# Kernel tuning notes

Measured on AMD Instinct MI355X. Metric: run time of the kernel, lower is better.

The kernel has to match this reference:

```python
import jax, jax.numpy as jnp
import numpy as np

D_MODEL = 512
H = 8
D_FF = 2048
EPS = 1e-6
NEG_INF = -1.0e9


def setup_inputs() -> dict:
    key = jax.random.key(0)
    ks = jax.random.split(key, 12)
    B, S, D, F = 8, 2048, D_MODEL, D_FF
    s = 0.02
    inp = {
        "x": jax.random.normal(ks[0], (B, S, D), jnp.float32),
        "src_mask": jnp.ones((B, 1, 1, S), jnp.int32),
        "w_q": jax.random.normal(ks[1], (D, D), jnp.float32) * s,
        "b_q": jnp.zeros((D,), jnp.float32),
        "w_k": jax.random.normal(ks[2], (D, D), jnp.float32) * s,
        "b_k": jnp.zeros((D,), jnp.float32),
        "w_v": jax.random.normal(ks[3], (D, D), jnp.float32) * s,
        "b_v": jnp.zeros((D,), jnp.float32),
        "w_o": jax.random.normal(ks[4], (D, D), jnp.float32) * s,
        "b_o": jnp.zeros((D,), jnp.float32),
        "w_1": jax.random.normal(ks[5], (F, D), jnp.float32) * s,
        "b_1": jnp.zeros((F,), jnp.float32),
        "w_2": jax.random.normal(ks[6], (D, F), jnp.float32) * s,
        "b_2": jnp.zeros((D,), jnp.float32),
    }
    return inp


def _layer_norm(x):
    # Matches torch: (x - mu) / sqrt(std**2 + eps), std is UNBIASED (ddof=1);
    # alpha/bias params exist in the module but are never applied in forward.
    mu = jnp.mean(x, axis=-1, keepdims=True)
    var = jnp.var(x, axis=-1, keepdims=True, ddof=1)
    return (x - mu) / jnp.sqrt(var + EPS)


def _mha(x, src_mask, w_q, b_q, w_k, b_k, w_v, b_v, w_o, b_o):
    B, S, D = x.shape
    d_k = D // H
    q = x @ w_q.T + b_q
    k = x @ w_k.T + b_k
    v = x @ w_v.T + b_v
    # (B, S, H, d_k) -> (B, H, S, d_k)
    q = q.reshape(B, S, H, d_k).transpose(0, 2, 1, 3)
    k = k.reshape(B, S, H, d_k).transpose(0, 2, 1, 3)
    v = v.reshape(B, S, H, d_k).transpose(0, 2, 1, 3)
    scores = jnp.einsum("bhqd,bhkd->bhqk", q, k) / jnp.sqrt(jnp.float32(d_k))
    scores = jnp.where(src_mask == 0, NEG_INF, scores)
    attn = jax.nn.softmax(scores, axis=-1)  # (B, H, S, S) materialized, as in source
    out = jnp.einsum("bhqk,bhkd->bhqd", attn, v)
    out = out.transpose(0, 2, 1, 3).reshape(B, S, D)
    return out @ w_o.T + b_o


def _ffn(x, w_1, b_1, w_2, b_2):
    return jax.nn.relu(x @ w_1.T + b_1) @ w_2.T + b_2


def reference(x, src_mask, w_q, b_q, w_k, b_k, w_v, b_v, w_o, b_o, w_1, b_1, w_2, b_2):
    # dropout prob = 0.0 -> identity (eval-equivalent)
    x1 = x + _mha(_layer_norm(x), src_mask, w_q, b_q, w_k, b_k, w_v, b_v, w_o, b_o)
    return x1 + _ffn(_layer_norm(x1), w_1, b_1, w_2, b_2)
```

## Files before the change

kernel.cpp:

```cpp
#include <hip/hip_runtime.h>
#include <hip/hip_bf16.h>

typedef unsigned short u16;
typedef __bf16 bf16x8 __attribute__((ext_vector_type(8)));
typedef unsigned int u32x4 __attribute__((ext_vector_type(4)));
typedef float f32x4 __attribute__((ext_vector_type(4)));

#define SEQ 2048
#define DMODEL 512
#define NHEAD 8
#define DFF 2048
#define NBATCH 8
#define MROWS (NBATCH * SEQ)

#define C1_FOLD 0.18033688f

__device__ __forceinline__ u16 f2b(float f) {
    __hip_bfloat16 h = __float2bfloat16(f);
    u16 u;
    __builtin_memcpy(&u, &h, 2);
    return u;
}

__device__ __forceinline__ unsigned int pack2(float a, float b) {
    float2 f{a, b};
    __hip_bfloat162 h = __float22bfloat162_rn(f);
    unsigned int u;
    __builtin_memcpy(&u, &h, 4);
    return u;
}

__device__ __forceinline__ float ex2(float x) {
#if __has_builtin(__builtin_amdgcn_exp2f)
    return __builtin_amdgcn_exp2f(x);
#else
    return exp2f(x);
#endif
}

__device__ __forceinline__ void gload_lds16(const void* g, void* lds) {
    auto* gp = reinterpret_cast<const __attribute__((address_space(1))) unsigned int*>(
        reinterpret_cast<uintptr_t>(g));
    auto* lp = reinterpret_cast<__attribute__((address_space(3))) unsigned int*>(
        reinterpret_cast<uintptr_t>(lds));
    __builtin_amdgcn_global_load_lds(gp, lp, 16, 0, 0);
}

__global__ __launch_bounds__(256) void cast_weights(
    const float* __restrict__ w0, const float* __restrict__ w1,
    const float* __restrict__ w2, const float* __restrict__ w3,
    const float* __restrict__ w4, const float* __restrict__ w5,
    u16* __restrict__ d0, u16* __restrict__ d1, u16* __restrict__ d2,
    u16* __restrict__ d3, u16* __restrict__ d4, u16* __restrict__ d5) {
    int blk = blockIdx.x;
    const float* s;
    u16* d;
    int base;
    float sc = 1.0f;
    if (blk < 512) {
        int seg = blk >> 7, lb = blk & 127;
        s = seg == 0 ? w0 : seg == 1 ? w1 : seg == 2 ? w2 : w3;
        d = seg == 0 ? d0 : seg == 1 ? d1 : seg == 2 ? d2 : d3;
        base = lb * 2048;
        if (seg == 0) sc = C1_FOLD;
    } else if (blk < 1024) {
        s = w4; d = d4; base = (blk - 512) * 2048;
    } else {
        s = w5; d = d5; base = (blk - 1024) * 2048;
    }
    int i = base + threadIdx.x * 8;
    float4 a = *reinterpret_cast<const float4*>(s + i);
    float4 b = *reinterpret_cast<const float4*>(s + i + 4);
    ushort4 oa, ob;
    oa.x = f2b(a.x * sc); oa.y = f2b(a.y * sc);
    oa.z = f2b(a.z * sc); oa.w = f2b(a.w * sc);
    ob.x = f2b(b.x * sc); ob.y = f2b(b.y * sc);
    ob.z = f2b(b.z * sc); ob.w = f2b(b.w * sc);
    *reinterpret_cast<ushort4*>(d + i) = oa;
    *reinterpret_cast<ushort4*>(d + i + 4) = ob;
}

__global__ __launch_bounds__(256) void concat_bias(const float* __restrict__ bq,
                                                   const float* __restrict__ bk,
                                                   const float* __restrict__ bv,
                                                   float* __restrict__ dst) {
    int i = blockIdx.x * 256 + threadIdx.x;
    float v = i < 512 ? bq[i] * C1_FOLD : (i < 1024 ? bk[i - 512] : bv[i - 1024]);
    dst[i] = v;
}

__global__ __launch_bounds__(256) void ln_rows(const float* __restrict__ x,
                                               u16* __restrict__ out) {
    int row = blockIdx.x * 4 + (threadIdx.x >> 6);
    int l = threadIdx.x & 63;
    const float* xr = x + (size_t)row * DMODEL + l * 8;
    float4 a = *reinterpret_cast<const float4*>(xr);
    float4 b = *reinterpret_cast<const float4*>(xr + 4);
    float s = a.x + a.y + a.z + a.w + b.x + b.y + b.z + b.w;
    float q = a.x * a.x + a.y * a.y + a.z * a.z + a.w * a.w +
              b.x * b.x + b.y * b.y + b.z * b.z + b.w * b.w;
#pragma unroll
    for (int d = 32; d >= 1; d >>= 1) {
        s += __shfl_xor(s, d, 64);
        q += __shfl_xor(q, d, 64);
    }
    float mean = s * (1.f / 512.f);
    float var = (q - 512.f * mean * mean) * (1.f / 511.f);
    float rs = rsqrtf(var + 1e-6f);
    ushort4 o0, o1;
    o0.x = f2b((a.x - mean) * rs); o0.y = f2b((a.y - mean) * rs);
    o0.z = f2b((a.z - mean) * rs); o0.w = f2b((a.w - mean) * rs);
    o1.x = f2b((b.x - mean) * rs); o1.y = f2b((b.y - mean) * rs);
    o1.z = f2b((b.z - mean) * rs); o1.w = f2b((b.w - mean) * rs);
    u16* op = out + (size_t)row * DMODEL + l * 8;
    *reinterpret_cast<ushort4*>(op) = o0;
    *reinterpret_cast<ushort4*>(op + 4) = o1;
}

template <bool RELU, bool RESID, int OUTMODE>
__global__ __launch_bounds__(256, 2) void gemm_nt(
    const u16* __restrict__ A, const u16* __restrict__ W,
    const float* __restrict__ bias, const float* __restrict__ resid,
    void* __restrict__ Cout, void* __restrict__ Cout2, int N, int K) {
    __shared__ u16 Als[2][128 * 64];
    __shared__ u16 Bls[2][128 * 64];
    const int tid = threadIdx.x;
    const int l = tid & 63, w = tid >> 6;
    const int m0 = blockIdx.y * 128;
    const int n0 = blockIdx.x * 128;
    const int wr = (w >> 1) * 64, wc = (w & 1) * 64;
    const int lhi = l >> 4, l15 = l & 15, l7 = l & 7;

    f32x4 acc[4][4] = {};

    const int srow = l >> 3;
    const int scol = ((l & 7) * 8) ^ (srow << 3);

    auto stage = [&](int buf, int kt) {
#pragma unroll
        for (int i = 0; i < 4; ++i) {
            int cc = w * 4 + i;
            int grow = cc * 8 + srow;
            gload_lds16(&A[(size_t)(m0 + grow) * K + kt + scol],
                        &Als[buf][cc * 512]);
            gload_lds16(&W[(size_t)(n0 + grow) * K + kt + scol],
                        &Bls[buf][cc * 512]);
        }
    };

    auto compute = [&](int buf) {
#pragma unroll
        for (int kk = 0; kk < 2; ++kk) {
            const int koff = (kk * 32 + lhi * 8) ^ (l7 << 3);
            bf16x8 af[4], bfr[4];
#pragma unroll
            for (int m = 0; m < 4; ++m)
                af[m] = *reinterpret_cast<const bf16x8*>(
                    &Als[buf][(wr + m * 16 + l15) * 64 + koff]);
#pragma unroll
            for (int n = 0; n < 4; ++n)
                bfr[n] = *reinterpret_cast<const bf16x8*>(
                    &Bls[buf][(wc + n * 16 + l15) * 64 + koff]);
#pragma unroll
            for (int m = 0; m < 4; ++m)
#pragma unroll
                for (int n = 0; n < 4; ++n)
                    acc[m][n] = __builtin_amdgcn_mfma_f32_16x16x32_bf16(
                        af[m], bfr[n], acc[m][n], 0, 0, 0);
        }
    };

    stage(0, 0);
    asm volatile("s_waitcnt vmcnt(0)" ::: "memory");
    __builtin_amdgcn_s_barrier();

    for (int kt = 0; kt < K; kt += 128) {
        if (kt + 64 < K) stage(1, kt + 64);
        __builtin_amdgcn_sched_barrier(0);
        compute(0);
        asm volatile("s_waitcnt vmcnt(0)" ::: "memory");
        __builtin_amdgcn_s_barrier();
        if (kt + 128 < K) stage(0, kt + 128);
        __builtin_amdgcn_sched_barrier(0);
        compute(1);
        asm volatile("s_waitcnt vmcnt(0)" ::: "memory");
        __builtin_amdgcn_s_barrier();
    }

    int colg[4];
    float bv[4];
#pragma unroll
    for (int cn = 0; cn < 4; ++cn) {
        colg[cn] = n0 + wc + cn * 16 + l15;
        bv[cn] = bias[colg[cn]];
    }
#pragma unroll
    for (int am = 0; am < 4; ++am) {
        int rowg = m0 + wr + am * 16 + 4 * lhi;
#pragma unroll
        for (int cn = 0; cn < 4; ++cn) {
            float v[4];
#pragma unroll
            for (int r = 0; r < 4; ++r) {
                float t = acc[am][cn][r] + bv[cn];
                if constexpr (RELU) t = fmaxf(t, 0.f);
                if constexpr (RESID)
                    t += resid[(size_t)(rowg + r) * N + colg[cn]];
                v[r] = t;
            }
            if constexpr (OUTMODE == 0) {
                u16* o = (u16*)Cout;
#pragma unroll
                for (int r = 0; r < 4; ++r)
                    o[(size_t)(rowg + r) * N + colg[cn]] = f2b(v[r]);
            } else if constexpr (OUTMODE == 1) {
                float* o = (float*)Cout;
#pragma unroll
                for (int r = 0; r < 4; ++r)
                    o[(size_t)(rowg + r) * N + colg[cn]] = v[r];
            } else {
                if (n0 < 1024) {
                    u16* o = (u16*)Cout;
#pragma unroll
                    for (int r = 0; r < 4; ++r)
                        o[(size_t)(rowg + r) * 1024 + colg[cn]] = f2b(v[r]);
                } else {
                    u16* o = (u16*)Cout2;
                    int bb = rowg >> 11, sloc = rowg & 2047;
                    int dg = colg[cn] - 1024;
                    int kk = sloc >> 5, hb = (sloc >> 4) & 1, ss = (sloc >> 2) & 3;
                    ushort4 pk;
                    pk.x = f2b(v[0]); pk.y = f2b(v[1]);
                    pk.z = f2b(v[2]); pk.w = f2b(v[3]);
                    *reinterpret_cast<ushort4*>(
                        &o[(size_t)(bb * 64 + kk) * 16384 + ss * 4096 + dg * 8 +
                           hb * 4]) = pk;
                }
            }
        }
    }
}

__global__ __launch_bounds__(256, 3) void attn_fwd(
    const u16* __restrict__ qk, const u16* __restrict__ v8,
    const int* __restrict__ mask, u16* __restrict__ out) {
    __shared__ u16 Kls[2][64 * 64];
    __shared__ u16 Vls[2][8 * 512];
    const int tid = threadIdx.x;
    const int l = tid & 63, w = tid >> 6;
    const int lhi = l >> 4, l15 = l & 15;
    const int lb = (blockIdx.x & 7) * 128 + (blockIdx.x >> 3);
    const int qt = lb & 15, bh = lb >> 4;
    const int b = bh >> 3, h = bh & 7;
    const int q0 = qt * 128 + w * 32;

    const u16* Qb = qk + (size_t)b * SEQ * 1024 + h * 64;
    const u16* Kb = Qb + 512;
    const u16* Vb8 = v8 + (size_t)b * 1048576 + h * 512;
    const int* Mb = mask + b * SEQ;

    const int srow = l >> 3;
    const int scol = ((l & 7) ^ srow) << 3;

    bf16x8 qf[2][2];
#pragma unroll
    for (int g = 0; g < 2; ++g) {
        size_t qa = (size_t)(q0 + g * 16 + l15) * 1024 + lhi * 8;
        qf[g][0] = *reinterpret_cast<const bf16x8*>(&Qb[qa]);
        qf[g][1] = *reinterpret_cast<const bf16x8*>(&Qb[qa + 32]);
    }

    bf16x8 ones8;
#pragma unroll
    for (int i = 0; i < 8; ++i) ones8[i] = (__bf16)1.0f;

    int allone;
    {
        int acc = 1;
#pragma unroll
        for (int i = 0; i < 8; ++i) {
            int4 mm = *reinterpret_cast<const int4*>(&Mb[l * 32 + i * 4]);
            acc &= mm.x & mm.y & mm.z & mm.w;
        }
        allone = __all(acc == 1);
    }

    f32x4 oacc[2][4] = {};
    f32x4 osum[2] = {};

    auto stage = [&](int buf, int kv) {
#pragma unroll
        for (int i = 0; i < 2; ++i) {
            int cc = w * 2 + i;
            int row = cc * 8 + srow;
            gload_lds16(&Kb[(size_t)(kv + row) * 1024 + scol], &Kls[buf][cc * 512]);
            gload_lds16(&Vb8[(size_t)((kv >> 5) + (cc >> 2)) * 16384 +
                             (cc & 3) * 4096 + l * 8],
                        &Vls[buf][cc * 512]);
        }
    };

    const int sw = (l15 & 7) << 3;

    auto tile = [&](int buf, int kv, bool pf, int pbuf, int pkv) {
        if (pf) stage(pbuf, pkv);
        __builtin_amdgcn_sched_barrier(0);

        f32x4 sc[2][4];
        __builtin_amdgcn_s_setprio(1);
#pragma unroll
        for (int ks = 0; ks < 4; ++ks) {
            int krow = ks * 16 + l15;
            bf16x8 ka0 = *reinterpret_cast<const bf16x8*>(
                &Kls[buf][krow * 64 + ((lhi * 8) ^ sw)]);
            bf16x8 ka1 = *reinterpret_cast<const bf16x8*>(
                &Kls[buf][krow * 64 + ((32 + lhi * 8) ^ sw)]);
#pragma unroll
            for (int g = 0; g < 2; ++g) {
                f32x4 z = {};
                z = __builtin_amdgcn_mfma_f32_16x16x32_bf16(ka0, qf[g][0], z, 0, 0, 0);
                z = __builtin_amdgcn_mfma_f32_16x16x32_bf16(ka1, qf[g][1], z, 0, 0, 0);
                sc[g][ks] = z;
            }
        }
        __builtin_amdgcn_s_setprio(0);

        if (!allone) {
            int4 mm[4];
#pragma unroll
            for (int ks = 0; ks < 4; ++ks)
                mm[ks] = *reinterpret_cast<const int4*>(&Mb[kv + ks * 16 + 4 * lhi]);
#pragma unroll
            for (int ks = 0; ks < 4; ++ks) {
                if (mm[ks].x == 0) { sc[0][ks][0] = -3e38f; sc[1][ks][0] = -3e38f; }
                if (mm[ks].y == 0) { sc[0][ks][1] = -3e38f; sc[1][ks][1] = -3e38f; }
                if (mm[ks].z == 0) { sc[0][ks][2] = -3e38f; sc[1][ks][2] = -3e38f; }
                if (mm[ks].w == 0) { sc[0][ks][3] = -3e38f; sc[1][ks][3] = -3e38f; }
            }
        }

        u32x4 pku[2][2];
#pragma unroll
        for (int g = 0; g < 2; ++g) {
#pragma unroll
            for (int ks = 0; ks < 4; ++ks) {
                float p0 = ex2(fminf(sc[g][ks][0], 30.f));
                float p1 = ex2(fminf(sc[g][ks][1], 30.f));
                float p2 = ex2(fminf(sc[g][ks][2], 30.f));
                float p3 = ex2(fminf(sc[g][ks][3], 30.f));
                pku[g][ks >> 1][(ks & 1) * 2 + 0] = pack2(p0, p1);
                pku[g][ks >> 1][(ks & 1) * 2 + 1] = pack2(p2, p3);
            }
        }

        __builtin_amdgcn_s_setprio(1);
#pragma unroll
        for (int kp = 0; kp < 2; ++kp) {
#pragma unroll
            for (int dc = 0; dc < 4; ++dc) {
                bf16x8 vb8 = *reinterpret_cast<const bf16x8*>(
                    &Vls[buf][(kp * 4 + lhi) * 512 + (dc * 16 + l15) * 8]);
#pragma unroll
                for (int g = 0; g < 2; ++g)
                    oacc[g][dc] = __builtin_amdgcn_mfma_f32_16x16x32_bf16(
                        __builtin_bit_cast(bf16x8, pku[g][kp]), vb8, oacc[g][dc],
                        0, 0, 0);
            }
#pragma unroll
            for (int g = 0; g < 2; ++g)
                osum[g] = __builtin_amdgcn_mfma_f32_16x16x32_bf16(
                    __builtin_bit_cast(bf16x8, pku[g][kp]), ones8, osum[g],
                    0, 0, 0);
        }
        __builtin_amdgcn_s_setprio(0);

        asm volatile("s_waitcnt vmcnt(0)" ::: "memory");
        __builtin_amdgcn_s_barrier();
    };

    stage(0, 0);
    asm volatile("s_waitcnt vmcnt(0)" ::: "memory");
    __builtin_amdgcn_s_barrier();

    for (int tt = 0; tt < 16; ++tt) {
        const int base = tt * 128;
        tile(0, base, true, 1, base + 64);
        tile(1, base + 64, tt < 15, 0, base + 128);
    }

#pragma unroll
    for (int g = 0; g < 2; ++g) {
#pragma unroll
        for (int r = 0; r < 4; ++r) {
            float inv = 1.f / osum[g][r];
            size_t rowa =
                ((size_t)b * SEQ + q0 + g * 16 + 4 * lhi + r) * DMODEL + h * 64;
#pragma unroll
            for (int dc = 0; dc < 4; ++dc)
                out[rowa + dc * 16 + l15] = f2b(oacc[g][dc][r] * inv);
        }
    }
}

extern "C" void kernel_launch(void* const* d_in, const int* in_sizes, int n_in,
                              void* d_out, int out_size, void* d_ws,
                              size_t ws_size, hipStream_t stream) {
    const float* x = (const float*)d_in[0];
    const int* mask = (const int*)d_in[1];
    const float* w_q = (const float*)d_in[2];
    const float* b_q = (const float*)d_in[3];
    const float* w_k = (const float*)d_in[4];
    const float* b_k = (const float*)d_in[5];
    const float* w_v = (const float*)d_in[6];
    const float* b_v = (const float*)d_in[7];
    const float* w_o = (const float*)d_in[8];
    const float* b_o = (const float*)d_in[9];
    const float* w_1 = (const float*)d_in[10];
    const float* b_1 = (const float*)d_in[11];
    const float* w_2 = (const float*)d_in[12];
    const float* b_2 = (const float*)d_in[13];

    char* ws = (char*)d_ws;
    const size_t MB = 1024ull * 1024ull;
    u16* lnx = (u16*)(ws + 0);
    u16* qkb = (u16*)(ws + 16 * MB);
    u16* v8 = (u16*)(ws + 48 * MB);
    u16* lnx1 = (u16*)(ws + 16 * MB);
    u16* hbuf = (u16*)(ws + 32 * MB);
    u16* wqkv = (u16*)(ws + 96 * MB);
    u16* wob = wqkv + 3 * 262144;
    u16* w1b = wqkv + 4 * 262144;
    u16* w2b = w1b + 1048576;
    float* bqkv = (float*)(w2b + 1048576);
    u16* attn_o = lnx;
    float* x1 = (float*)d_out;

    cast_weights<<<1536, 256, 0, stream>>>(
        w_q, w_k, w_v, w_o, w_1, w_2, wqkv, wqkv + 262144, wqkv + 2 * 262144,
        wob, w1b, w2b);
    concat_bias<<<6, 256, 0, stream>>>(b_q, b_k, b_v, bqkv);
    ln_rows<<<4096, 256, 0, stream>>>(x, lnx);

    dim3 g12(12, 128), g4(4, 128), g16(16, 128);
    gemm_nt<false, false, 3><<<g12, 256, 0, stream>>>(lnx, wqkv, bqkv, nullptr,
                                                      qkb, v8, 1536, 512);
    attn_fwd<<<1024, 256, 0, stream>>>(qkb, v8, mask, attn_o);
    gemm_nt<false, true, 1><<<g4, 256, 0, stream>>>(attn_o, wob, b_o, x, x1,
                                                    nullptr, 512, 512);
    ln_rows<<<4096, 256, 0, stream>>>(x1, lnx1);
    gemm_nt<true, false, 0><<<g16, 256, 0, stream>>>(lnx1, w1b, b_1, nullptr,
                                                     hbuf, nullptr, 2048, 512);
    gemm_nt<false, true, 1><<<g4, 256, 0, stream>>>(hbuf, w2b, b_2, x1,
                                                    (float*)d_out, nullptr,
                                                    512, 2048);
}
```

Before: 269.6 us.

## Add 256x256-tile 8-wave GEMM with phased pipelining for QKV and FFN1

New measurement: 271.6 us. About the same (+0.7%).

```diff
diff --git a/kernel.cpp b/kernel.cpp
--- a/kernel.cpp
+++ b/kernel.cpp
@@ -117,6 +117,141 @@
     *reinterpret_cast<ushort4*>(op + 4) = o1;
 }
 
+template <bool RELU, int OUTMODE>
+__global__ __launch_bounds__(512, 2) void gemm256(
+    const u16* __restrict__ A, const u16* __restrict__ W,
+    const float* __restrict__ bias,
+    void* __restrict__ Cout, void* __restrict__ Cout2, int N, int K) {
+    __shared__ u16 LS[2][2][2][8192];
+    const int tid = threadIdx.x;
+    const int l = tid & 63, w = tid >> 6;
+    const int l15 = l & 15, lhi = l >> 4;
+    const int m0 = blockIdx.y * 256, n0 = blockIdx.x * 256;
+    const int wr = (w >> 2) * 128;
+    const int wc = (w & 3) * 64;
+
+    f32x4 acc[8][4] = {};
+
+    const int goff = (4 * l15 + (lhi ^ ((l15 >> 1) & 3))) * 8;
+    const int sgran = ((l & 3) ^ ((l >> 3) & 3)) * 8;
+    const int srow = l >> 2;
+
+    auto stageH = [&](int q, int kh, int mat, int ktn) {
+#pragma unroll
+        for (int i = 0; i < 2; ++i) {
+            int c = 2 * w + i;
+            const u16* src =
+                (mat == 0 ? A : W) +
+                (size_t)((mat == 0 ? m0 : n0) + c * 16 + srow) * K + ktn +
+                kh * 32 + sgran;
+            gload_lds16(src, &LS[q][kh][mat][c * 512]);
+        }
+    };
+
+    bf16x8 bq[4];
+
+    auto phase = [&](int p, int kh, int mh, int stcode, int ktn, int vm) {
+        if (stcode >= 0) stageH(p ^ 1, stcode >> 1, stcode & 1, ktn);
+        if (vm == 6) asm volatile("s_waitcnt vmcnt(6)" ::: "memory");
+        else if (vm == 4) asm volatile("s_waitcnt vmcnt(4)" ::: "memory");
+        else if (vm == 0) asm volatile("s_waitcnt vmcnt(0)" ::: "memory");
+        bf16x8 aq[4];
+        if (mh == 0) {
+#pragma unroll
+            for (int nf = 0; nf < 4; ++nf)
+                bq[nf] = *reinterpret_cast<const bf16x8*>(
+                    &LS[p][kh][1][((wc >> 4) + nf) * 512 + goff]);
+        }
+#pragma unroll
+        for (int mf = 0; mf < 4; ++mf)
+            aq[mf] = *reinterpret_cast<const bf16x8*>(
+                &LS[p][kh][0][((wr >> 4) + mh * 4 + mf) * 512 + goff]);
+        __builtin_amdgcn_s_barrier();
+        asm volatile("s_waitcnt lgkmcnt(0)" ::: "memory");
+        __builtin_amdgcn_sched_barrier(0);
+        __builtin_amdgcn_s_setprio(1);
+#pragma unroll
+        for (int mf = 0; mf < 4; ++mf)
+#pragma unroll
+            for (int nf = 0; nf < 4; ++nf)
+                acc[mh * 4 + mf][nf] = __builtin_amdgcn_mfma_f32_16x16x32_bf16(
+                    aq[mf], bq[nf], acc[mh * 4 + mf][nf], 0, 0, 0);
+        __builtin_amdgcn_s_setprio(0);
+        __builtin_amdgcn_s_barrier();
+    };
+
+    auto tileF = [&](int p, int kt, bool pf) {
+        int ktn = kt + 64;
+        phase(p, 0, 0, pf ? 0 : -1, ktn, pf ? 6 : 4);
+        phase(p, 0, 1, pf ? 1 : -1, ktn, -1);
+        phase(p, 1, 0, pf ? 2 : -1, ktn, pf ? 6 : 0);
+        phase(p, 1, 1, pf ? 3 : -1, ktn, -1);
+    };
+
+    stageH(0, 0, 0, 0);
+    stageH(0, 0, 1, 0);
+    stageH(0, 1, 0, 0);
+    stageH(0, 1, 1, 0);
+    asm volatile("s_waitcnt vmcnt(0)" ::: "memory");
+    __builtin_amdgcn_s_barrier();
+
+    const int nt = K >> 6;
+    int kt = 0;
+    for (int tt = 0; tt < (nt >> 1) - 1; ++tt) {
+        tileF(0, kt, true);
+        tileF(1, kt + 64, true);
+        kt += 128;
+    }
+    tileF(0, kt, true);
+    tileF(1, kt + 64, false);
+
+    int colg[4];
+    float bv[4];
+#pragma unroll
+    for (int nf = 0; nf < 4; ++nf) {
+        colg[nf] = n0 + wc + nf * 16 + l15;
+        bv[nf] = bias[colg[nf]];
+    }
+#pragma unroll
+    for (int mf = 0; mf < 8; ++mf) {
+        int rowg = m0 + wr + mf * 16 + 4 * lhi;
+#pragma unroll
+        for (int nf = 0; nf < 4; ++nf) {
+            float v[4];
+#pragma unroll
+            for (int r = 0; r < 4; ++r) {
+                float t = acc[mf][nf][r] + bv[nf];
+                if constexpr (RELU) t = fmaxf(t, 0.f);
+                v[r] = t;
+            }
+            if constexpr (OUTMODE == 0) {
+                u16* o = (u16*)Cout;
+#pragma unroll
+                for (int r = 0; r < 4; ++r)
+                    o[(size_t)(rowg + r) * N + colg[nf]] = f2b(v[r]);
+            } else {
+                if (n0 < 1024) {
+                    u16* o = (u16*)Cout;
+#pragma unroll
+                    for (int r = 0; r < 4; ++r)
+                        o[(size_t)(rowg + r) * 1024 + colg[nf]] = f2b(v[r]);
+                } else {
+                    u16* o = (u16*)Cout2;
+                    int bb = rowg >> 11, sloc = rowg & 2047;
+                    int dg = colg[nf] - 1024;
+                    int kk = sloc >> 5, hb = (sloc >> 4) & 1, ss = (sloc >> 2) & 3;
+                    ushort4 pk;
+                    pk.x = f2b(v[0]); pk.y = f2b(v[1]);
+                    pk.z = f2b(v[2]); pk.w = f2b(v[3]);
+                    *reinterpret_cast<ushort4*>(
+                        &o[(size_t)(bb * 64 + kk) * 16384 + ss * 4096 + dg * 8 +
+                           hb * 4]) = pk;
+                }
+            }
+        }
+    }
+}
+
 template <bool RELU, bool RESID, int OUTMODE>
 __global__ __launch_bounds__(256, 2) void gemm_nt(
     const u16* __restrict__ A, const u16* __restrict__ W,
@@ -213,29 +348,11 @@
 #pragma unroll
                 for (int r = 0; r < 4; ++r)
                     o[(size_t)(rowg + r) * N + colg[cn]] = f2b(v[r]);
-            } else if constexpr (OUTMODE == 1) {
+            } else {
                 float* o = (float*)Cout;
 #pragma unroll
                 for (int r = 0; r < 4; ++r)
                     o[(size_t)(rowg + r) * N + colg[cn]] = v[r];
-            } else {
-                if (n0 < 1024) {
-                    u16* o = (u16*)Cout;
-#pragma unroll
-                    for (int r = 0; r < 4; ++r)
-                        o[(size_t)(rowg + r) * 1024 + colg[cn]] = f2b(v[r]);
-                } else {
-                    u16* o = (u16*)Cout2;
-                    int bb = rowg >> 11, sloc = rowg & 2047;
-                    int dg = colg[cn] - 1024;
-                    int kk = sloc >> 5, hb = (sloc >> 4) & 1, ss = (sloc >> 2) & 3;
-                    ushort4 pk;
-                    pk.x = f2b(v[0]); pk.y = f2b(v[1]);
-                    pk.z = f2b(v[2]); pk.w = f2b(v[3]);
-                    *reinterpret_cast<ushort4*>(
-                        &o[(size_t)(bb * 64 + kk) * 16384 + ss * 4096 + dg * 8 +
-                           hb * 4]) = pk;
-                }
             }
         }
     }
@@ -441,16 +558,14 @@
     concat_bias<<<6, 256, 0, stream>>>(b_q, b_k, b_v, bqkv);
     ln_rows<<<4096, 256, 0, stream>>>(x, lnx);
 
-    dim3 g12(12, 128), g4(4, 128), g16(16, 128);
-    gemm_nt<false, false, 3><<<g12, 256, 0, stream>>>(lnx, wqkv, bqkv, nullptr,
-                                                      qkb, v8, 1536, 512);
+    gemm256<false, 3><<<dim3(6, 64), 512, 0, stream>>>(lnx, wqkv, bqkv, qkb,
+                                                       v8, 1536, 512);
     attn_fwd<<<1024, 256, 0, stream>>>(qkb, v8, mask, attn_o);
-    gemm_nt<false, true, 1><<<g4, 256, 0, stream>>>(attn_o, wob, b_o, x, x1,
-                                                    nullptr, 512, 512);
+    gemm_nt<false, true, 1><<<dim3(4, 128), 256, 0, stream>>>(
+        attn_o, wob, b_o, x, x1, nullptr, 512, 512);
     ln_rows<<<4096, 256, 0, stream>>>(x1, lnx1);
-    gemm_nt<true, false, 0><<<g16, 256, 0, stream>>>(lnx1, w1b, b_1, nullptr,
-                                                     hbuf, nullptr, 2048, 512);
-    gemm_nt<false, true, 1><<<g4, 256, 0, stream>>>(hbuf, w2b, b_2, x1,
-                                                    (float*)d_out, nullptr,
-                                                    512, 2048);
-}
+    gemm256<true, 0><<<dim3(8, 64), 512, 0, stream>>>(lnx1, w1b, b_1, hbuf,
+                                                      nullptr, 2048, 512);
+    gemm_nt<false, true, 1><<<dim3(4, 128), 256, 0, stream>>>(
+        hbuf, w2b, b_2, x1, (float*)d_out, nullptr, 512, 2048);
+}
```
